# Kernel optimization log

Hardware: AMD Instinct MI355X
Metric: run time of the kernel (lower is better)

The kernel has to match this reference:

```python
import jax, jax.numpy as jnp
import numpy as np

B = 32       # batch
IN_N = 32    # input capsules
IN_D = 16    # input capsule dim (== out_d)
H = 14       # input spatial
OUT_N = 32   # output capsules
OUT_D = 16
HO = 7       # parent grid h_out = w_out
HID = 64     # Linformer projection dim
EPS = 1e-5


def _gconv(x, w, groups):
    # x: [b, C, H, W], w: [C_out, C_in/groups, kh, kw]; stride 1, pad 1
    return jax.lax.conv_general_dilated(
        x, w, window_strides=(1, 1), padding=((1, 1), (1, 1)),
        dimension_numbers=("NCHW", "OIHW", "NCHW"), feature_group_count=groups)


def setup_inputs() -> dict:
    key = jax.random.key(0)
    ks = jax.random.split(key, 7)
    current_pose = jax.random.normal(ks[0], (B, IN_N, H, H, IN_D), dtype=jnp.float32)
    next_pose = jax.random.normal(ks[1], (B, OUT_N, HO, HO, OUT_D), dtype=jnp.float32)
    # grouped conv weights (torch layout OIHW, groups = IN_N)
    current_w = 0.05 * jax.random.normal(ks[2], (IN_N * IN_D, IN_D, 3, 3), dtype=jnp.float32)
    next_w = 0.05 * jax.random.normal(ks[3], (OUT_N * OUT_D, OUT_N * OUT_D // IN_N, 3, 3), dtype=jnp.float32)
    E_proj = 0.02 * jax.random.normal(ks[4], (IN_N, H * H, HID), dtype=jnp.float32)
    rel_embedd = jax.random.normal(ks[5], (IN_D, HO * HO), dtype=jnp.float32)
    ln_gamma = jnp.ones((OUT_D,), dtype=jnp.float32)
    ln_beta = jnp.zeros((OUT_D,), dtype=jnp.float32)
    return {
        "current_pose": current_pose, "next_pose": next_pose,
        "current_w": current_w, "next_w": next_w,
        "E_proj": E_proj, "rel_embedd": rel_embedd,
        "ln_gamma": ln_gamma, "ln_beta": ln_beta,
        "num_iter": 1,
    }


def reference(current_pose, next_pose, current_w, next_w, E_proj, rel_embedd,
              ln_gamma, ln_beta, num_iter):
    b = current_pose.shape[0]
    # 5D -> [b, n*d, H, W]
    cp = current_pose.transpose(0, 2, 3, 1, 4).reshape(b, H, H, IN_N * IN_D)
    cp = cp.transpose(0, 3, 1, 2)
    cp = _gconv(cp, current_w, IN_N)                       # [b, n*d, H, H]
    # headwise Linformer key projection
    cp = cp.reshape(b, IN_D, IN_N, 1, H * H)
    k = jnp.matmul(cp, E_proj)                             # [b, d, n, 1, HID]
    k = k.reshape(b, IN_D, IN_N * HID).transpose(0, 2, 1)  # [b, n*HID, d]
    rel = jnp.broadcast_to(rel_embedd.T[None], (b, HO * HO, IN_D))
    k = jnp.concatenate([k, rel], axis=1)                  # [b, N, d]

    # parent pose -> queries
    q = next_pose.transpose(0, 2, 3, 1, 4).reshape(b, HO, HO, OUT_N * OUT_D)
    q = q.transpose(0, 3, 1, 2)
    q = _gconv(q, next_w, IN_N)                            # [b, out_n*out_d, HO, HO]
    q = q.reshape(b, OUT_N * HO * HO, OUT_D)               # [b, J, d]

    dots = jnp.einsum("bje,bie->bji", q, k) * (IN_D ** -0.5)  # [b, J, N]
    dots = jax.nn.softmax(dots, axis=-2)                   # softmax over queries j
    out = jnp.einsum("bji,bie->bje", dots, k)              # [b, J, d]

    out = out.reshape(b, OUT_N * IN_D, HO, HO)
    out = _gconv(out, next_w, IN_N)
    out = out.reshape(b, OUT_N, HO, HO, IN_D)

    # LayerNorm over last dim (dropout rate = 0)
    mu = out.mean(-1, keepdims=True)
    var = ((out - mu) ** 2).mean(-1, keepdims=True)
    out = (out - mu) / jnp.sqrt(var + EPS) * ln_gamma + ln_beta
    return out
```

## Files before the change

kernel.cpp:

```cpp
#include <hip/hip_runtime.h>

typedef unsigned short u16;
typedef __attribute__((ext_vector_type(8))) short short8;
typedef __attribute__((ext_vector_type(4))) float floatx4;
typedef __attribute__((ext_vector_type(4))) unsigned uintx4;

#define MFMA16(a, b, c) __builtin_amdgcn_mfma_f32_16x16x32_bf16(a, b, c, 0, 0, 0)

__device__ inline u16 bf16rn(float x) {
    unsigned u = __float_as_uint(x);
    u += 0x7fffu + ((u >> 16) & 1u);
    return (u16)(u >> 16);
}
__device__ inline float bf16tof(u16 h) { return __uint_as_float(((unsigned)h) << 16); }
__device__ inline short8 ld8(const u16* p) { return *(const short8*)p; }
__device__ inline unsigned pack2(float a, float b) {
    return __builtin_amdgcn_perm(__float_as_uint(b), __float_as_uint(a), 0x07060302u);
}

__global__ __launch_bounds__(256) void k_ecvt2(const float* __restrict__ E,
                                               const float* __restrict__ rel,
                                               const float* __restrict__ w,
                                               u16* __restrict__ EhT,
                                               u16* __restrict__ ElT,
                                               u16* __restrict__ Kh,
                                               u16* __restrict__ Kl,
                                               u16* __restrict__ KhT,
                                               u16* __restrict__ KlT,
                                               float* __restrict__ w2) {
    int blk = blockIdx.x, tid = threadIdx.x;
    if (blk < 32) {
        __shared__ float ep[196 * 65];
        int m = blk;
        const float* eb = E + (size_t)m * 12544;
        for (int t = tid; t < 12544; t += 256) {
            int p = t >> 6, h = t & 63;
            ep[p * 65 + h] = eb[t];
        }
        __syncthreads();
        for (int t = tid; t < 64 * 224; t += 256) {
            int h = t / 224, p = t % 224;
            float v = (p < 196) ? ep[p * 65 + h] : 0.f;
            u16 hi = bf16rn(v);
            u16 lo = bf16rn(v - bf16tof(hi));
            EhT[(size_t)m * 14336 + t] = hi;
            ElT[(size_t)m * 14336 + t] = lo;
        }
    } else if (blk < 64) {
        int b = blk - 32;
        size_t bK = (size_t)b * 2112;
        size_t bT = (size_t)b * 33792;
#pragma unroll
        for (int k = 0; k < 4; ++k) {
            int idx = tid + k * 256;
            int row = idx >> 4, e = idx & 15;
            int i = 2048 + row;
            float v = (row < 49) ? rel[e * 49 + row] : 0.f;
            u16 h = bf16rn(v);
            u16 l = bf16rn(v - bf16tof(h));
            Kh[(bK + i) * 16 + e] = h;
            Kl[(bK + i) * 16 + e] = l;
            KhT[bT + (size_t)e * 2112 + i] = h;
            KlT[bT + (size_t)e * 2112 + i] = l;
        }
    } else {
        int g0 = (blk - 64) * 4;
        for (int t = tid; t < 4 * 2304; t += 256) {
            int g = g0 + t / 2304, r = t % 2304;
            int oc = r / 144, rr = r % 144;
            w2[(size_t)g * 2304 + (rr / 9) * 144 + oc * 9 + (rr % 9)] =
                w[(size_t)g * 2304 + r];
        }
    }
}

__global__ __launch_bounds__(256) void k_conv14(const float* __restrict__ pose,
                                                const float* __restrict__ w2,
                                                float* __restrict__ out) {
    int blk = blockIdx.x;
    int oh = blk & 1, bg = blk >> 1;
    int tid = threadIdx.x;
    __shared__ float patch[16 * 256];
#pragma unroll
    for (int k = 0; k < 16; ++k) patch[k * 256 + tid] = 0.f;
    __syncthreads();
    const float* pin = pose + (size_t)bg * 3136;
    for (int t = tid; t < 3136; t += 256) {
        int p = t >> 4, ic = t & 15;
        int y = p / 14, x = p % 14;
        patch[ic * 256 + (y + 1) * 16 + (x + 1)] = pin[t];
    }
    __syncthreads();
    int g = bg & 31;
    const float* wg = w2 + (size_t)g * 2304 + oh * 72;
    float* po = out + (size_t)bg * 3136 + oh * 8 * 196;
    if (tid < 196) {
        int y = tid / 14, x = tid % 14;
        int base = (y + 1) * 16 + (x + 1);
        float acc[8];
#pragma unroll
        for (int oc = 0; oc < 8; ++oc) acc[oc] = 0.f;
        for (int ic = 0; ic < 16; ++ic) {
            const float* pr = patch + ic * 256 + base;
            float win[9];
#pragma unroll
            for (int ky = 0; ky < 3; ++ky)
#pragma unroll
                for (int kx = 0; kx < 3; ++kx)
                    win[ky * 3 + kx] = pr[(ky - 1) * 16 + (kx - 1)];
            const float* wi = wg + ic * 144;
#pragma unroll
            for (int oc = 0; oc < 8; ++oc)
#pragma unroll
                for (int kk = 0; kk < 9; ++kk)
                    acc[oc] += win[kk] * wi[oc * 9 + kk];
        }
#pragma unroll
        for (int oc = 0; oc < 8; ++oc) po[oc * 196 + tid] = acc[oc];
    }
}

__global__ __launch_bounds__(64) void k_conv7(const float* __restrict__ in,
                                              const float* __restrict__ in2,
                                              const float* __restrict__ w,
                                              float* __restrict__ out, int mode) {
    int blk = blockIdx.x;
    int oh = blk & 1, bg = blk >> 1;
    int tid = threadIdx.x;
    __shared__ float patch[16 * 144];
    for (int t = tid; t < 16 * 144; t += 64) patch[t] = 0.f;
    __syncthreads();
    const float* pin = in + (size_t)bg * 784;
    if (mode == 1) {
        for (int t = tid; t < 784; t += 64) {
            int p = t >> 4, ic = t & 15;
            int y = p / 7, x = p % 7;
            patch[ic * 144 + (y + 1) * 16 + (x + 1)] = pin[t];
        }
    } else {
        const float* pin2 = in2 + (size_t)bg * 784;
        for (int t = tid; t < 784; t += 64) {
            int ic = t / 49, p = t % 49;
            int y = p / 7, x = p % 7;
            patch[ic * 144 + (y + 1) * 16 + (x + 1)] =
                (pin[t] + pin[t + 802816]) + (pin2[t] + pin2[t + 802816]);
        }
    }
    __syncthreads();
    int g = bg & 31;
    const float* wg = w + (size_t)g * 2304 + (size_t)oh * 8 * 144;
    float* po = out + (size_t)bg * 784 + (size_t)oh * 8 * 49;
    if (tid < 49) {
        int y = tid / 7, x = tid % 7;
        int base = (y + 1) * 16 + (x + 1);
        float acc[8];
#pragma unroll
        for (int oc = 0; oc < 8; ++oc) acc[oc] = 0.f;
        for (int ic = 0; ic < 16; ++ic) {
            const float* pr = patch + ic * 144 + base;
            float win[9];
#pragma unroll
            for (int ky = 0; ky < 3; ++ky)
#pragma unroll
                for (int kx = 0; kx < 3; ++kx)
                    win[ky * 3 + kx] = pr[(ky - 1) * 16 + (kx - 1)];
            const float* wi = wg + ic * 9;
#pragma unroll
            for (int oc = 0; oc < 8; ++oc)
#pragma unroll
                for (int kk = 0; kk < 9; ++kk)
                    acc[oc] += win[kk] * wi[oc * 144 + kk];
        }
#pragma unroll
        for (int oc = 0; oc < 8; ++oc) po[oc * 49 + tid] = acc[oc];
    }
}

__global__ __launch_bounds__(256) void k_kproj2(const float* __restrict__ cpconv,
                                                const u16* __restrict__ EhT,
                                                const u16* __restrict__ ElT,
                                                u16* __restrict__ Kh,
                                                u16* __restrict__ Kl,
                                                u16* __restrict__ KhT,
                                                u16* __restrict__ KlT) {
    int blk = blockIdx.x;
    int b = blk >> 5, m = blk & 31;
    int wave = threadIdx.x >> 6, lane = threadIdx.x & 63;
    int ht = wave;
    int n = lane & 15, quad = lane >> 4;

    const float* arow = cpconv + ((size_t)b * 512 + (size_t)n * 32 + m) * 196;
    const u16* bhrow = EhT + ((size_t)m * 64 + ht * 16 + n) * 224;
    const u16* blrow = ElT + ((size_t)m * 64 + ht * 16 + n) * 224;

    floatx4 c = {0.f, 0.f, 0.f, 0.f};
#pragma unroll
    for (int pc = 0; pc < 7; ++pc) {
        int p0 = pc * 32 + quad * 8;
        float av[8];
        if (p0 <= 188) {
            float4 x = *(const float4*)(arow + p0);
            float4 y = *(const float4*)(arow + p0 + 4);
            av[0]=x.x; av[1]=x.y; av[2]=x.z; av[3]=x.w;
            av[4]=y.x; av[5]=y.y; av[6]=y.z; av[7]=y.w;
        } else {
#pragma unroll
            for (int k2 = 0; k2 < 8; ++k2) av[k2] = (p0 + k2 < 196) ? arow[p0 + k2] : 0.f;
        }
        short8 ah, al;
#pragma unroll
        for (int k2 = 0; k2 < 8; ++k2) {
            u16 h = bf16rn(av[k2]);
            ah[k2] = (short)h;
            al[k2] = (short)bf16rn(av[k2] - bf16tof(h));
        }
        short8 bh = ld8(bhrow + pc * 32 + quad * 8);
        short8 bl = ld8(blrow + pc * 32 + quad * 8);
        c = MFMA16(ah, bh, c);
        c = MFMA16(ah, bl, c);
        c = MFMA16(al, bh, c);
    }
    int i = m * 64 + ht * 16 + n;
    size_t bK = (size_t)b * 2112;
    size_t bT = (size_t)b * 33792;
    u16 h[4], l[4];
#pragma unroll
    for (int r = 0; r < 4; ++r) {
        h[r] = bf16rn(c[r]);
        l[r] = bf16rn(c[r] - bf16tof(h[r]));
    }
    *(uint2*)(Kh + (bK + i) * 16 + quad * 4) =
        make_uint2((unsigned)h[0] | ((unsigned)h[1] << 16), (unsigned)h[2] | ((unsigned)h[3] << 16));
    *(uint2*)(Kl + (bK + i) * 16 + quad * 4) =
        make_uint2((unsigned)l[0] | ((unsigned)l[1] << 16), (unsigned)l[2] | ((unsigned)l[3] << 16));
#pragma unroll
    for (int r = 0; r < 4; ++r) {
        KhT[bT + (size_t)(quad * 4 + r) * 2112 + i] = h[r];
        KlT[bT + (size_t)(quad * 4 + r) * 2112 + i] = l[r];
    }
}

__global__ __launch_bounds__(256) void k_cvt(const float* __restrict__ qconv,
                                             u16* __restrict__ Qp) {
    int gid = blockIdx.x * 256 + threadIdx.x;
    const float4* q4 = (const float4*)(qconv + (size_t)gid * 16);
    float4 t0 = q4[0], t1 = q4[1], t2 = q4[2], t3 = q4[3];
    float v[16] = {t0.x,t0.y,t0.z,t0.w, t1.x,t1.y,t1.z,t1.w,
                   t2.x,t2.y,t2.z,t2.w, t3.x,t3.y,t3.z,t3.w};
    unsigned hw[8], lw[8];
#pragma unroll
    for (int t = 0; t < 8; ++t) {
        float x0 = v[2*t] * 0.25f, x1 = v[2*t+1] * 0.25f;
        u16 h0 = bf16rn(x0), h1 = bf16rn(x1);
        u16 l0 = bf16rn(x0 - bf16tof(h0)), l1 = bf16rn(x1 - bf16tof(h1));
        hw[t] = (unsigned)h0 | ((unsigned)h1 << 16);
        lw[t] = (unsigned)l0 | ((unsigned)l1 << 16);
    }
    uint4* r4 = (uint4*)(Qp + (size_t)gid * 32);
    r4[0] = make_uint4(hw[0], hw[1], hw[2], hw[3]);
    r4[1] = make_uint4(hw[4], hw[5], hw[6], hw[7]);
    r4[2] = make_uint4(lw[0], lw[1], lw[2], lw[3]);
    r4[3] = make_uint4(lw[4], lw[5], lw[6], lw[7]);
}

__global__ __launch_bounds__(256) void k_stats4(const u16* __restrict__ Qp,
                                                const u16* __restrict__ Kh,
                                                const u16* __restrict__ Kl,
                                                float* __restrict__ dpart) {
    int blk = blockIdx.x;
    int b = blk / 34; int rem = blk % 34; int jh = rem / 17; int tb = rem % 17;
    int wave = threadIdx.x >> 6, lane = threadIdx.x & 63;
    int it2 = tb * 4 + wave;
    if (it2 >= 66) return;
    int ibase = it2 * 32;
    int n = lane & 15, quad = lane >> 4;
    size_t bK = (size_t)b * 2112;
    const u16* kb = Kh + (bK + ibase + n) * 16 + (quad & 1) * 8;
    const u16* lb = Kl + (bK + ibase + n) * 16 + (quad & 1) * 8;
    short8 bh0 = ld8(kb), bh1 = ld8(kb + 256);
    short8 bl0 = ld8(lb), bl1 = ld8(lb + 256);
    const u16* qb = Qp + (size_t)b * 50176 + (size_t)jh * 49 * 512 + n * 32 + quad * 8;
    floatx4 d0 = {0.f,0.f,0.f,0.f}, d1 = {0.f,0.f,0.f,0.f};
    short8 a0 = ld8(qb), a1 = ld8(qb + 512);
    for (int c = 0; c < 49; ++c) {
        short8 a2 = (c + 2 < 49) ? ld8(qb + (size_t)(c + 2) * 512) : a0;
        floatx4 s0 = {0.f,0.f,0.f,0.f}, s1 = {0.f,0.f,0.f,0.f};
        s0 = MFMA16(a0, bh0, s0);
        s0 = MFMA16(a0, bl0, s0);
        s1 = MFMA16(a0, bh1, s1);
        s1 = MFMA16(a0, bl1, s1);
        d0.x += __expf(s0.x); d0.y += __expf(s0.y);
        d0.z += __expf(s0.z); d0.w += __expf(s0.w);
        d1.x += __expf(s1.x); d1.y += __expf(s1.y);
        d1.z += __expf(s1.z); d1.w += __expf(s1.w);
        a0 = a1; a1 = a2;
    }
    float t0 = d0.x + d0.y + d0.z + d0.w;
    float t1 = d1.x + d1.y + d1.z + d1.w;
    t0 += __shfl_xor(t0, 16); t0 += __shfl_xor(t0, 32);
    t1 += __shfl_xor(t1, 16); t1 += __shfl_xor(t1, 32);
    if (quad == 0) {
        dpart[(size_t)jh * 67584 + bK + ibase + n]      = t0;
        dpart[(size_t)jh * 67584 + bK + ibase + 16 + n] = t1;
    }
}

__global__ __launch_bounds__(256) void k_vscale(const float* __restrict__ dpart,
                                                u16* __restrict__ VhT,
                                                u16* __restrict__ VlT) {
    int gid = blockIdx.x * 256 + threadIdx.x;
    int ic = gid % 264;
    int be = gid / 264;
    int b = be >> 4, e = be & 15;
    size_t off = (size_t)b * 33792 + (size_t)e * 2112 + (size_t)ic * 8;
    short8 h8 = ld8(VhT + off);
    short8 l8 = ld8(VlT + off);
    const float* dp = dpart + (size_t)b * 2112 + ic * 8;
    float4 da0 = *(const float4*)dp;
    float4 da1 = *(const float4*)(dp + 4);
    float4 db0 = *(const float4*)(dp + 67584);
    float4 db1 = *(const float4*)(dp + 67588);
    float d[8] = {da0.x+db0.x, da0.y+db0.y, da0.z+db0.z, da0.w+db0.w,
                  da1.x+db1.x, da1.y+db1.y, da1.z+db1.z, da1.w+db1.w};
    short8 oh, ol;
#pragma unroll
    for (int k = 0; k < 8; ++k) {
        float v = bf16tof((u16)h8[k]) + bf16tof((u16)l8[k]);
        float sv = v / d[k];
        u16 hh = bf16rn(sv);
        ol[k] = (short)bf16rn(sv - bf16tof(hh));
        oh[k] = (short)hh;
    }
    *(short8*)(VhT + off) = oh;
    *(short8*)(VlT + off) = ol;
}

__global__ __launch_bounds__(256) void k_pv8(const u16* __restrict__ Qp,
                                             const u16* __restrict__ Kh,
                                             const u16* __restrict__ Kl,
                                             const u16* __restrict__ VhT,
                                             const u16* __restrict__ VlT,
                                             float* __restrict__ opart) {
    __shared__ __align__(16) u16 sH[2][32][16];
    __shared__ __align__(16) u16 sL[2][32][16];
    __shared__ __align__(16) u16 tH[2][16][32];
    __shared__ __align__(16) u16 tL[2][16][32];

    int blk = blockIdx.x;
    int b = blk / 52; int rem = blk % 52; int jtb = rem >> 2; int iq = rem & 3;
    int tid = threadIdx.x, wave = tid >> 6, lane = tid & 63;
    int n = lane & 15, quad = lane >> 4, qh = quad & 1;
    int jt0 = (jtb * 4 + wave) * 2;
    int jc0 = jt0     < 98 ? jt0     : 97;
    int jc1 = jt0 + 1 < 98 ? jt0 + 1 : 97;
    int nc = (iq < 2) ? 17 : 16;
    int i0 = iq * 512 + (iq < 2 ? iq : 2) * 32;
    size_t bK = (size_t)b * 2112;
    size_t bT = (size_t)b * 33792;

    short8 aq0 = ld8(Qp + ((size_t)b * 1568 + (size_t)jc0 * 16 + n) * 32 + quad * 8);
    short8 aq1 = ld8(Qp + ((size_t)b * 1568 + (size_t)jc1 * 16 + n) * 32 + quad * 8);

    int role = wave, L = lane;
    uint4 sreg;
    auto ldchunk = [&](int c) {
        int i0c = i0 + c * 32;
        if (role == 0)      sreg = *(const uint4*)(Kh  + (bK + i0c + (L >> 1)) * 16 + (L & 1) * 8);
        else if (role == 1) sreg = *(const uint4*)(Kl  + (bK + i0c + (L >> 1)) * 16 + (L & 1) * 8);
        else if (role == 2) sreg = *(const uint4*)(VhT + bT + (size_t)(L >> 2) * 2112 + i0c + (L & 3) * 8);
        else                sreg = *(const uint4*)(VlT + bT + (size_t)(L >> 2) * 2112 + i0c + (L & 3) * 8);
    };
    auto stchunk = [&](int bf) {
        if (role == 0)      *(uint4*)(&sH[bf][L >> 1][(L & 1) * 8]) = sreg;
        else if (role == 1) *(uint4*)(&sL[bf][L >> 1][(L & 1) * 8]) = sreg;
        else if (role == 2) *(uint4*)(&tH[bf][L >> 2][(L & 3) * 8]) = sreg;
        else                *(uint4*)(&tL[bf][L >> 2][(L & 3) * 8]) = sreg;
    };

    floatx4 o0 = {0.f, 0.f, 0.f, 0.f}, o1 = {0.f, 0.f, 0.f, 0.f};

    ldchunk(0); stchunk(0); ldchunk(1);
    __syncthreads();
    for (int c = 0; c < nc; ++c) {
        int cb = c & 1;
        short8 sh0 = ld8(&sH[cb][n][qh * 8]);
        short8 sh1 = ld8(&sH[cb][16 + n][qh * 8]);
        short8 sl0 = ld8(&sL[cb][n][qh * 8]);
        short8 sl1 = ld8(&sL[cb][16 + n][qh * 8]);
        short8 th  = ld8(&tH[cb][n][quad * 8]);
        short8 tl  = ld8(&tL[cb][n][quad * 8]);

        {
            floatx4 s0 = {0.f,0.f,0.f,0.f}, s1 = {0.f,0.f,0.f,0.f};
            s0 = MFMA16(sh0, aq0, s0);
            s0 = MFMA16(sl0, aq0, s0);
            s1 = MFMA16(sh1, aq0, s1);
            s1 = MFMA16(sl1, aq0, s1);
            unsigned u00 = pack2(__expf(s0[0]), __expf(s0[1]));
            unsigned u01 = pack2(__expf(s0[2]), __expf(s0[3]));
            unsigned u10 = pack2(__expf(s1[0]), __expf(s1[1]));
            unsigned u11 = pack2(__expf(s1[2]), __expf(s1[3]));
            asm("v_permlane32_swap_b32 %0, %1" : "+v"(u00), "+v"(u10));
            asm("v_permlane32_swap_b32 %0, %1" : "+v"(u01), "+v"(u11));
            asm("v_permlane16_swap_b32 %0, %1" : "+v"(u00), "+v"(u10));
            asm("v_permlane16_swap_b32 %0, %1" : "+v"(u01), "+v"(u11));
            uintx4 uv = {u00, u01, u10, u11};
            short8 aw = __builtin_bit_cast(short8, uv);
            o0 = MFMA16(aw, th, o0);
            o0 = MFMA16(aw, tl, o0);
        }
        {
            floatx4 s0 = {0.f,0.f,0.f,0.f}, s1 = {0.f,0.f,0.f,0.f};
            s0 = MFMA16(sh0, aq1, s0);
            s0 = MFMA16(sl0, aq1, s0);
            s1 = MFMA16(sh1, aq1, s1);
            s1 = MFMA16(sl1, aq1, s1);
            unsigned u00 = pack2(__expf(s0[0]), __expf(s0[1]));
            unsigned u01 = pack2(__expf(s0[2]), __expf(s0[3]));
            unsigned u10 = pack2(__expf(s1[0]), __expf(s1[1]));
            unsigned u11 = pack2(__expf(s1[2]), __expf(s1[3]));
            asm("v_permlane32_swap_b32 %0, %1" : "+v"(u00), "+v"(u10));
            asm("v_permlane32_swap_b32 %0, %1" : "+v"(u01), "+v"(u11));
            asm("v_permlane16_swap_b32 %0, %1" : "+v"(u00), "+v"(u10));
            asm("v_permlane16_swap_b32 %0, %1" : "+v"(u01), "+v"(u11));
            uintx4 uv = {u00, u01, u10, u11};
            short8 aw = __builtin_bit_cast(short8, uv);
            o1 = MFMA16(aw, th, o1);
            o1 = MFMA16(aw, tl, o1);
        }
        if (c + 1 < nc) stchunk((c + 1) & 1);
        if (c + 2 < nc) ldchunk(c + 2);
        __syncthreads();
    }
    if (jt0 < 98) {
        float* ob = opart + (size_t)iq * 802816 +
                    ((size_t)b * 1568 + (size_t)jt0 * 16) * 16;
#pragma unroll
        for (int r = 0; r < 4; ++r) ob[(quad * 4 + r) * 16 + n] = o0[r];
    }
    if (jt0 + 1 < 98) {
        float* ob = opart + (size_t)iq * 802816 +
                    ((size_t)b * 1568 + (size_t)(jt0 + 1) * 16) * 16;
#pragma unroll
        for (int r = 0; r < 4; ++r) ob[(quad * 4 + r) * 16 + n] = o1[r];
    }
}

__global__ __launch_bounds__(256) void k_ln(const float* __restrict__ x,
                                            const float* __restrict__ gamma,
                                            const float* __restrict__ beta,
                                            float* __restrict__ out, int ngroups) {
    int g = blockIdx.x * 256 + threadIdx.x;
    if (g >= ngroups) return;
    const float4* xp = (const float4*)(x + (size_t)g * 16);
    float4 x0 = xp[0], x1 = xp[1], x2 = xp[2], x3 = xp[3];
    float sum = x0.x + x0.y + x0.z + x0.w + x1.x + x1.y + x1.z + x1.w
              + x2.x + x2.y + x2.z + x2.w + x3.x + x3.y + x3.z + x3.w;
    float mu = sum * 0.0625f;
    float var = 0.f;
    var += (x0.x-mu)*(x0.x-mu) + (x0.y-mu)*(x0.y-mu) + (x0.z-mu)*(x0.z-mu) + (x0.w-mu)*(x0.w-mu);
    var += (x1.x-mu)*(x1.x-mu) + (x1.y-mu)*(x1.y-mu) + (x1.z-mu)*(x1.z-mu) + (x1.w-mu)*(x1.w-mu);
    var += (x2.x-mu)*(x2.x-mu) + (x2.y-mu)*(x2.y-mu) + (x2.z-mu)*(x2.z-mu) + (x2.w-mu)*(x2.w-mu);
    var += (x3.x-mu)*(x3.x-mu) + (x3.y-mu)*(x3.y-mu) + (x3.z-mu)*(x3.z-mu) + (x3.w-mu)*(x3.w-mu);
    float rstd = rsqrtf(var * 0.0625f + 1e-5f);
    const float4* gp = (const float4*)gamma;
    const float4* bp = (const float4*)beta;
    float4 g0 = gp[0], g1 = gp[1], g2 = gp[2], g3 = gp[3];
    float4 be0 = bp[0], be1 = bp[1], be2 = bp[2], be3 = bp[3];
    float4 o0, o1, o2, o3;
    o0.x = (x0.x-mu)*rstd*g0.x + be0.x; o0.y = (x0.y-mu)*rstd*g0.y + be0.y;
    o0.z = (x0.z-mu)*rstd*g0.z + be0.z; o0.w = (x0.w-mu)*rstd*g0.w + be0.w;
    o1.x = (x1.x-mu)*rstd*g1.x + be1.x; o1.y = (x1.y-mu)*rstd*g1.y + be1.y;
    o1.z = (x1.z-mu)*rstd*g1.z + be1.z; o1.w = (x1.w-mu)*rstd*g1.w + be1.w;
    o2.x = (x2.x-mu)*rstd*g2.x + be2.x; o2.y = (x2.y-mu)*rstd*g2.y + be2.y;
    o2.z = (x2.z-mu)*rstd*g2.z + be2.z; o2.w = (x2.w-mu)*rstd*g2.w + be2.w;
    o3.x = (x3.x-mu)*rstd*g3.x + be3.x; o3.y = (x3.y-mu)*rstd*g3.y + be3.y;
    o3.z = (x3.z-mu)*rstd*g3.z + be3.z; o3.w = (x3.w-mu)*rstd*g3.w + be3.w;
    float4* op = (float4*)(out + (size_t)g * 16);
    op[0] = o0; op[1] = o1; op[2] = o2; op[3] = o3;
}

extern "C" void kernel_launch(void* const* d_in, const int* in_sizes, int n_in,
                              void* d_out, int out_size, void* d_ws, size_t ws_size,
                              hipStream_t stream) {
    const float* current_pose = (const float*)d_in[0];
    const float* next_pose    = (const float*)d_in[1];
    const float* current_w    = (const float*)d_in[2];
    const float* next_w       = (const float*)d_in[3];
    const float* E_proj       = (const float*)d_in[4];
    const float* rel          = (const float*)d_in[5];
    const float* ln_gamma     = (const float*)d_in[6];
    const float* ln_beta      = (const float*)d_in[7];
    float* out = (float*)d_out;
    float* ws  = (float*)d_ws;

    float* cpconv = ws;
    float* opart  = ws;
    float* qconv  = ws + 3211264;
    float* dpart  = qconv;
    float* conv2  = qconv;
    float* w2     = ws + 4014080;
    u16*   ub     = (u16*)(ws + 4087808);
    u16* Qp  = ub;
    u16* Kh  = ub + 1605632;
    u16* Kl  = ub + 2686976;
    u16* KhT = ub + 3768320;
    u16* KlT = ub + 4849664;
    u16* EhT = ub + 5931008;
    u16* ElT = ub + 6389760;

    k_ecvt2 <<<72,   256, 0, stream>>>(E_proj, rel, current_w, EhT, ElT,
                                       Kh, Kl, KhT, KlT, w2);
    k_conv14<<<2048, 256, 0, stream>>>(current_pose, w2, cpconv);
    k_conv7 <<<2048, 64,  0, stream>>>(next_pose, next_pose, next_w, qconv, 1);
    k_cvt   <<<196,  256, 0, stream>>>(qconv, Qp);
    k_kproj2<<<1024, 256, 0, stream>>>(cpconv, EhT, ElT, Kh, Kl, KhT, KlT);
    k_stats4<<<1088, 256, 0, stream>>>(Qp, Kh, Kl, dpart);
    k_vscale<<<528,  256, 0, stream>>>(dpart, KhT, KlT);
    k_pv8   <<<1664, 256, 0, stream>>>(Qp, Kh, Kl, KhT, KlT, opart);
    k_conv7 <<<2048, 64,  0, stream>>>(opart, opart + 1605632, next_w, conv2, 0);
    k_ln    <<<196,  256, 0, stream>>>(conv2, ln_gamma, ln_beta, out, 50176);
}
```

Measured before the change: 225.2 us.

## Fuse query conv with bf16 split and output conv with LayerNorm

Folds the bf16 hi/lo conversion into the 7x7 query grouped-conv kernel, and folds the LayerNorm into the output grouped-conv kernel. Each block now handles all 16 output channels of one (batch, group) with two waves and stages results through padded shared memory. This removes two launches and the fp32 round trip through global memory for qconv and conv2. In exchange it halves the block count and makes only 49 threads do the epilogue, with extra shared-memory sync.

New measurement: 232.5 us. 3.2% more time.

```diff
diff --git a/kernel.cpp b/kernel.cpp
--- a/kernel.cpp
+++ b/kernel.cpp
@@ -17,6 +17,8 @@
 __device__ inline unsigned pack2(float a, float b) {
     return __builtin_amdgcn_perm(__float_as_uint(b), __float_as_uint(a), 0x07060302u);
 }
+
+#define FOIDX(i) ((i) + ((i) >> 4))
 
 __global__ __launch_bounds__(256) void k_ecvt2(const float* __restrict__ E,
                                                const float* __restrict__ rel,
@@ -120,38 +122,27 @@
     }
 }
 
-__global__ __launch_bounds__(64) void k_conv7(const float* __restrict__ in,
-                                              const float* __restrict__ in2,
-                                              const float* __restrict__ w,
-                                              float* __restrict__ out, int mode) {
+__global__ __launch_bounds__(128) void k_qconv(const float* __restrict__ pose,
+                                               const float* __restrict__ w,
+                                               u16* __restrict__ Qp) {
     int blk = blockIdx.x;
-    int oh = blk & 1, bg = blk >> 1;
+    int b = blk >> 5, g = blk & 31;
     int tid = threadIdx.x;
     __shared__ float patch[16 * 144];
-    for (int t = tid; t < 16 * 144; t += 64) patch[t] = 0.f;
-    __syncthreads();
-    const float* pin = in + (size_t)bg * 784;
-    if (mode == 1) {
-        for (int t = tid; t < 784; t += 64) {
-            int p = t >> 4, ic = t & 15;
-            int y = p / 7, x = p % 7;
-            patch[ic * 144 + (y + 1) * 16 + (x + 1)] = pin[t];
-        }
-    } else {
-        const float* pin2 = in2 + (size_t)bg * 784;
-        for (int t = tid; t < 784; t += 64) {
-            int ic = t / 49, p = t % 49;
-            int y = p / 7, x = p % 7;
-            patch[ic * 144 + (y + 1) * 16 + (x + 1)] =
-                (pin[t] + pin[t + 802816]) + (pin2[t] + pin2[t + 802816]);
-        }
-    }
-    __syncthreads();
-    int g = bg & 31;
-    const float* wg = w + (size_t)g * 2304 + (size_t)oh * 8 * 144;
-    float* po = out + (size_t)bg * 784 + (size_t)oh * 8 * 49;
-    if (tid < 49) {
-        int y = tid / 7, x = tid % 7;
+    __shared__ float fo[833];
+    for (int t = tid; t < 16 * 144; t += 128) patch[t] = 0.f;
+    __syncthreads();
+    const float* pin = pose + (size_t)blk * 784;
+    for (int t = tid; t < 784; t += 128) {
+        int p = t >> 4, ic = t & 15;
+        int y = p / 7, x = p % 7;
+        patch[ic * 144 + (y + 1) * 16 + (x + 1)] = pin[t];
+    }
+    __syncthreads();
+    int oh = tid >> 6, lane = tid & 63;
+    if (lane < 49) {
+        const float* wg = w + (size_t)g * 2304 + (size_t)oh * 8 * 144;
+        int y = lane / 7, x = lane % 7;
         int base = (y + 1) * 16 + (x + 1);
         float acc[8];
 #pragma unroll
@@ -172,7 +163,99 @@
                     acc[oc] += win[kk] * wi[oc * 144 + kk];
         }
 #pragma unroll
-        for (int oc = 0; oc < 8; ++oc) po[oc * 49 + tid] = acc[oc];
+        for (int oc = 0; oc < 8; ++oc)
+            fo[FOIDX((oh * 8 + oc) * 49 + lane)] = acc[oc];
+    }
+    __syncthreads();
+    if (tid < 49) {
+        float v[16];
+#pragma unroll
+        for (int k = 0; k < 16; ++k) v[k] = fo[FOIDX(tid * 16 + k)];
+        unsigned hw[8], lw[8];
+#pragma unroll
+        for (int t = 0; t < 8; ++t) {
+            float x0 = v[2 * t] * 0.25f, x1 = v[2 * t + 1] * 0.25f;
+            u16 h0 = bf16rn(x0), h1 = bf16rn(x1);
+            u16 l0 = bf16rn(x0 - bf16tof(h0)), l1 = bf16rn(x1 - bf16tof(h1));
+            hw[t] = (unsigned)h0 | ((unsigned)h1 << 16);
+            lw[t] = (unsigned)l0 | ((unsigned)l1 << 16);
+        }
+        uint4* r4 = (uint4*)(Qp + ((size_t)b * 1568 + (size_t)g * 49 + tid) * 32);
+        r4[0] = make_uint4(hw[0], hw[1], hw[2], hw[3]);
+        r4[1] = make_uint4(hw[4], hw[5], hw[6], hw[7]);
+        r4[2] = make_uint4(lw[0], lw[1], lw[2], lw[3]);
+        r4[3] = make_uint4(lw[4], lw[5], lw[6], lw[7]);
+    }
+}
+
+__global__ __launch_bounds__(128) void k_oconv(const float* __restrict__ in,
+                                               const float* __restrict__ w,
+                                               const float* __restrict__ gamma,
+                                               const float* __restrict__ beta,
+                                               float* __restrict__ out) {
+    int blk = blockIdx.x;
+    int g = blk & 31;
+    int tid = threadIdx.x;
+    __shared__ float patch[16 * 144];
+    __shared__ float fo[833];
+    for (int t = tid; t < 16 * 144; t += 128) patch[t] = 0.f;
+    __syncthreads();
+    const float* pin = in + (size_t)blk * 784;
+    for (int t = tid; t < 784; t += 128) {
+        int ic = t / 49, p = t % 49;
+        int y = p / 7, x = p % 7;
+        patch[ic * 144 + (y + 1) * 16 + (x + 1)] =
+            (pin[t] + pin[t + 802816]) + (pin[t + 1605632] + pin[t + 2408448]);
+    }
+    __syncthreads();
+    int oh = tid >> 6, lane = tid & 63;
+    if (lane < 49) {
+        const float* wg = w + (size_t)g * 2304 + (size_t)oh * 8 * 144;
+        int y = lane / 7, x = lane % 7;
+        int base = (y + 1) * 16 + (x + 1);
+        float acc[8];
+#pragma unroll
+        for (int oc = 0; oc < 8; ++oc) acc[oc] = 0.f;
+        for (int ic = 0; ic < 16; ++ic) {
+            const float* pr = patch + ic * 144 + base;
+            float win[9];
+#pragma unroll
+            for (int ky = 0; ky < 3; ++ky)
+#pragma unroll
+                for (int kx = 0; kx < 3; ++kx)
+                    win[ky * 3 + kx] = pr[(ky - 1) * 16 + (kx - 1)];
+            const float* wi = wg + ic * 9;
+#pragma unroll
+            for (int oc = 0; oc < 8; ++oc)
+#pragma unroll
+                for (int kk = 0; kk < 9; ++kk)
+                    acc[oc] += win[kk] * wi[oc * 144 + kk];
+        }
+#pragma unroll
+        for (int oc = 0; oc < 8; ++oc)
+            fo[FOIDX((oh * 8 + oc) * 49 + lane)] = acc[oc];
+    }
+    __syncthreads();
+    if (tid < 49) {
+        float v[16];
+#pragma unroll
+        for (int k = 0; k < 16; ++k) v[k] = fo[FOIDX(tid * 16 + k)];
+        float sum = 0.f;
+#pragma unroll
+        for (int k = 0; k < 16; ++k) sum += v[k];
+        float mu = sum * 0.0625f;
+        float var = 0.f;
+#pragma unroll
+        for (int k = 0; k < 16; ++k) var += (v[k] - mu) * (v[k] - mu);
+        float rstd = rsqrtf(var * 0.0625f + 1e-5f);
+        float o[16];
+#pragma unroll
+        for (int k = 0; k < 16; ++k) o[k] = (v[k] - mu) * rstd * gamma[k] + beta[k];
+        float4* op = (float4*)(out + (size_t)blk * 784 + (size_t)tid * 16);
+        op[0] = make_float4(o[0], o[1], o[2], o[3]);
+        op[1] = make_float4(o[4], o[5], o[6], o[7]);
+        op[2] = make_float4(o[8], o[9], o[10], o[11]);
+        op[3] = make_float4(o[12], o[13], o[14], o[15]);
     }
 }
 
@@ -238,29 +321,6 @@
         KhT[bT + (size_t)(quad * 4 + r) * 2112 + i] = h[r];
         KlT[bT + (size_t)(quad * 4 + r) * 2112 + i] = l[r];
     }
-}
-
-__global__ __launch_bounds__(256) void k_cvt(const float* __restrict__ qconv,
-                                             u16* __restrict__ Qp) {
-    int gid = blockIdx.x * 256 + threadIdx.x;
-    const float4* q4 = (const float4*)(qconv + (size_t)gid * 16);
-    float4 t0 = q4[0], t1 = q4[1], t2 = q4[2], t3 = q4[3];
-    float v[16] = {t0.x,t0.y,t0.z,t0.w, t1.x,t1.y,t1.z,t1.w,
-                   t2.x,t2.y,t2.z,t2.w, t3.x,t3.y,t3.z,t3.w};
-    unsigned hw[8], lw[8];
-#pragma unroll
-    for (int t = 0; t < 8; ++t) {
-        float x0 = v[2*t] * 0.25f, x1 = v[2*t+1] * 0.25f;
-        u16 h0 = bf16rn(x0), h1 = bf16rn(x1);
-        u16 l0 = bf16rn(x0 - bf16tof(h0)), l1 = bf16rn(x1 - bf16tof(h1));
-        hw[t] = (unsigned)h0 | ((unsigned)h1 << 16);
-        lw[t] = (unsigned)l0 | ((unsigned)l1 << 16);
-    }
-    uint4* r4 = (uint4*)(Qp + (size_t)gid * 32);
-    r4[0] = make_uint4(hw[0], hw[1], hw[2], hw[3]);
-    r4[1] = make_uint4(hw[4], hw[5], hw[6], hw[7]);
-    r4[2] = make_uint4(lw[0], lw[1], lw[2], lw[3]);
-    r4[3] = make_uint4(lw[4], lw[5], lw[6], lw[7]);
 }
 
 __global__ __launch_bounds__(256) void k_stats4(const u16* __restrict__ Qp,
@@ -446,40 +506,6 @@
     }
 }
 
-__global__ __launch_bounds__(256) void k_ln(const float* __restrict__ x,
-                                            const float* __restrict__ gamma,
-                                            const float* __restrict__ beta,
-                                            float* __restrict__ out, int ngroups) {
-    int g = blockIdx.x * 256 + threadIdx.x;
-    if (g >= ngroups) return;
-    const float4* xp = (const float4*)(x + (size_t)g * 16);
-    float4 x0 = xp[0], x1 = xp[1], x2 = xp[2], x3 = xp[3];
-    float sum = x0.x + x0.y + x0.z + x0.w + x1.x + x1.y + x1.z + x1.w
-              + x2.x + x2.y + x2.z + x2.w + x3.x + x3.y + x3.z + x3.w;
-    float mu = sum * 0.0625f;
-    float var = 0.f;
-    var += (x0.x-mu)*(x0.x-mu) + (x0.y-mu)*(x0.y-mu) + (x0.z-mu)*(x0.z-mu) + (x0.w-mu)*(x0.w-mu);
-    var += (x1.x-mu)*(x1.x-mu) + (x1.y-mu)*(x1.y-mu) + (x1.z-mu)*(x1.z-mu) + (x1.w-mu)*(x1.w-mu);
-    var += (x2.x-mu)*(x2.x-mu) + (x2.y-mu)*(x2.y-mu) + (x2.z-mu)*(x2.z-mu) + (x2.w-mu)*(x2.w-mu);
-    var += (x3.x-mu)*(x3.x-mu) + (x3.y-mu)*(x3.y-mu) + (x3.z-mu)*(x3.z-mu) + (x3.w-mu)*(x3.w-mu);
-    float rstd = rsqrtf(var * 0.0625f + 1e-5f);
-    const float4* gp = (const float4*)gamma;
-    const float4* bp = (const float4*)beta;
-    float4 g0 = gp[0], g1 = gp[1], g2 = gp[2], g3 = gp[3];
-    float4 be0 = bp[0], be1 = bp[1], be2 = bp[2], be3 = bp[3];
-    float4 o0, o1, o2, o3;
-    o0.x = (x0.x-mu)*rstd*g0.x + be0.x; o0.y = (x0.y-mu)*rstd*g0.y + be0.y;
-    o0.z = (x0.z-mu)*rstd*g0.z + be0.z; o0.w = (x0.w-mu)*rstd*g0.w + be0.w;
-    o1.x = (x1.x-mu)*rstd*g1.x + be1.x; o1.y = (x1.y-mu)*rstd*g1.y + be1.y;
-    o1.z = (x1.z-mu)*rstd*g1.z + be1.z; o1.w = (x1.w-mu)*rstd*g1.w + be1.w;
-    o2.x = (x2.x-mu)*rstd*g2.x + be2.x; o2.y = (x2.y-mu)*rstd*g2.y + be2.y;
-    o2.z = (x2.z-mu)*rstd*g2.z + be2.z; o2.w = (x2.w-mu)*rstd*g2.w + be2.w;
-    o3.x = (x3.x-mu)*rstd*g3.x + be3.x; o3.y = (x3.y-mu)*rstd*g3.y + be3.y;
-    o3.z = (x3.z-mu)*rstd*g3.z + be3.z; o3.w = (x3.w-mu)*rstd*g3.w + be3.w;
-    float4* op = (float4*)(out + (size_t)g * 16);
-    op[0] = o0; op[1] = o1; op[2] = o2; op[3] = o3;
-}
-
 extern "C" void kernel_launch(void* const* d_in, const int* in_sizes, int n_in,
                               void* d_out, int out_size, void* d_ws, size_t ws_size,
                               hipStream_t stream) {
@@ -496,9 +522,7 @@
 
     float* cpconv = ws;
     float* opart  = ws;
-    float* qconv  = ws + 3211264;
-    float* dpart  = qconv;
-    float* conv2  = qconv;
+    float* dpart  = ws + 3211264;
     float* w2     = ws + 4014080;
     u16*   ub     = (u16*)(ws + 4087808);
     u16* Qp  = ub;
@@ -512,12 +536,10 @@
     k_ecvt2 <<<72,   256, 0, stream>>>(E_proj, rel, current_w, EhT, ElT,
                                        Kh, Kl, KhT, KlT, w2);
     k_conv14<<<2048, 256, 0, stream>>>(current_pose, w2, cpconv);
-    k_conv7 <<<2048, 64,  0, stream>>>(next_pose, next_pose, next_w, qconv, 1);
-    k_cvt   <<<196,  256, 0, stream>>>(qconv, Qp);
+    k_qconv <<<1024, 128, 0, stream>>>(next_pose, next_w, Qp);
     k_kproj2<<<1024, 256, 0, stream>>>(cpconv, EhT, ElT, Kh, Kl, KhT, KlT);
     k_stats4<<<1088, 256, 0, stream>>>(Qp, Kh, Kl, dpart);
     k_vscale<<<528,  256, 0, stream>>>(dpart, KhT, KlT);
     k_pv8   <<<1664, 256, 0, stream>>>(Qp, Kh, Kl, KhT, KlT, opart);
-    k_conv7 <<<2048, 64,  0, stream>>>(opart, opart + 1605632, next_w, conv2, 0);
-    k_ln    <<<196,  256, 0, stream>>>(conv2, ln_gamma, ln_beta, out, 50176);
-}
+    k_oconv <<<1024, 128, 0, stream>>>(opart, next_w, ln_gamma, ln_beta, out);
+}
```
